# Performance work log

Measured on AMD Instinct MI355X. Metric: run time of the kernel, lower is better.

Reference implementation:

```python
import jax, jax.numpy as jnp
import numpy as np

B, S, I, H = 128, 1024, 512, 1024


def setup_inputs() -> dict:
    key = jax.random.key(0)
    k0, k1, k2 = jax.random.split(key, 3)
    scale = 0.02
    return {
        "x": jax.random.normal(k0, (B, S, I), jnp.float32),
        "feature_weighting": jnp.ones((1, 1, I), jnp.float32),
        "temporal_weighting": jnp.ones((1, S, 1), jnp.float32),
        "magnitude": jnp.ones((1,), jnp.float32),
        "W0": jax.random.normal(k1, (3 * H, I + H), jnp.float32) * scale,
        "b0": jnp.zeros((3 * H,), jnp.float32),
        "W1": jax.random.normal(k2, (3 * H, 2 * H), jnp.float32) * scale,
        "b1": jnp.zeros((3 * H,), jnp.float32),
    }


def _cell(x_t, h_prev, c_prev, W, b):
    # gates: [B, 3H] from cat(x, h_prev) @ W.T + b
    gates = jnp.concatenate([x_t, h_prev], axis=1) @ W.T + b
    i, g, o = jnp.split(gates, 3, axis=1)
    f = jax.nn.sigmoid(c_prev)            # note: forget gate from c_prev (module's quirk)
    c_new = f * c_prev + jax.nn.sigmoid(i) * jnp.tanh(g)
    h_new = jax.nn.sigmoid(o) * jnp.tanh(c_new) * f  # extra *f (module's quirk)
    return h_new, c_new


def reference(x, feature_weighting, temporal_weighting, magnitude, W0, b0, W1, b1):
    batch = x.shape[0]
    hid = W0.shape[0] // 3
    x = x * feature_weighting * temporal_weighting * jnp.exp(magnitude)
    zeros = jnp.zeros((batch, hid), x.dtype)
    init = (zeros, zeros, zeros, zeros)  # h0, c0, h1, c1

    def step(carry, x_t):
        h0, c0, h1, c1 = carry
        h0, c0 = _cell(x_t, h0, c0, W0, b0)
        h1, c1 = _cell(h0, h1, c1, W1, b1)
        return (h0, c0, h1, c1), h1

    (h0, c0, h1, c1), ys = jax.lax.scan(step, init, jnp.swapaxes(x, 0, 1))
    outputs = jnp.swapaxes(ys, 0, 1)  # [B, S, H]
    return outputs, ((h0, c0), (h1, c1))
```

## Files before the change

### kernel.cpp

```cpp
#include <hip/hip_runtime.h>
#include <hip/hip_bf16.h>


typedef __attribute__((ext_vector_type(8))) _Float16 f16x8;
typedef __attribute__((ext_vector_type(4))) float f32x4;
typedef unsigned long long u64;
#define DEV __device__ __forceinline__

namespace {
constexpr int Bb = 128, Ss = 1024, Ii = 512, Hh = 1024;
constexpr int K0 = Ii + Hh;
constexpr int K1 = 2 * Hh;
constexpr int NWG = 256;
constexpr int NPH = Ss + 1;
constexpr int RING = 16;
constexpr int LAG  = 12;
constexpr int SSTR = 32;

constexpr size_t BH    = (size_t)Bb * Hh;
constexpr size_t OF_H0 = (size_t)Bb * Ss * Hh;
constexpr size_t OF_C0 = OF_H0 + BH;
constexpr size_t OF_H1 = OF_C0 + BH;
constexpr size_t OF_C1 = OF_H1 + BH;

constexpr size_t WS_SLOTS = 4096;
constexpr size_t WS_C0    = 40960;
constexpr size_t WS_C1    = WS_C0 + BH * 4;
constexpr size_t RINGF    = (size_t)RING * BH * 2;
constexpr size_t WS_H0F   = WS_C1 + BH * 4;
constexpr size_t WS_H1F   = WS_H0F + RINGF;
constexpr size_t WS_ZEND  = WS_H1F + RINGF;
constexpr size_t WSZ_W0   = (size_t)3 * Hh * K0 * 2;
constexpr size_t WSZ_W1   = (size_t)3 * Hh * K1 * 2;
constexpr size_t WS_W0F   = WS_ZEND;
constexpr size_t WS_W1F   = WS_W0F + WSZ_W0;
constexpr size_t WS_NEED  = WS_W1F + WSZ_W1;

constexpr int CHUNKB    = 3072;
constexpr int LO_BYTES  = 48 * CHUNKB;
constexpr int RED_BYTES = 4 * 3 * 64 * 16;
constexpr int DYN_LDS   = LO_BYTES + RED_BYTES;
}

DEV unsigned short f16b(float f) {
  return __builtin_bit_cast(unsigned short, (_Float16)f);
}
DEV float sig_(float x) { return 1.f / (1.f + __expf(-x)); }
DEV float tanh_(float x) {
  float e = __expf(-2.f * fabsf(x));
  return copysignf((1.f - e) / (1.f + e), x);
}
DEV f16x8 ldh(const unsigned short* p) { return *reinterpret_cast<const f16x8*>(p); }
#define MFMAH __builtin_amdgcn_mfma_f32_16x16x32_f16

__global__ void k_zero(uint4* p, int n16) {
  for (int i = blockIdx.x * blockDim.x + threadIdx.x; i < n16; i += gridDim.x * blockDim.x)
    p[i] = make_uint4(0u, 0u, 0u, 0u);
}

__global__ void k_convert(const float* __restrict__ W0, const float* __restrict__ W1,
                          unsigned short* __restrict__ w0f, unsigned short* __restrict__ w1f) {
  const long NW04 = (long)3 * Hh * K0 / 4;
  const long NW14 = (long)3 * Hh * K1 / 4;
  const long total = NW04 + NW14;
  for (long i = (long)blockIdx.x * blockDim.x + threadIdx.x; i < total;
       i += (long)gridDim.x * blockDim.x) {
    long e; const float* src; unsigned short* dst;
    if (i < NW04) { e = i * 4;          src = W0 + e; dst = w0f + e; }
    else          { e = (i - NW04) * 4; src = W1 + e; dst = w1f + e; }
    f32x4 v = *(const f32x4*)src;
    u64 pk = 0;
#pragma unroll
    for (int e2 = 0; e2 < 4; ++e2) pk |= (u64)f16b(v[e2]) << (16 * e2);
    *(u64*)dst = pk;
  }
}

#define LD_WC(g, ch)                                                          \
  (*(const f16x8*)(lds + (ch) * CHUNKB + (g) * 1024 + l4 * 256 + l15 * 16))

#define HLOAD(arr, n, hP, kaB)                                                \
  _Pragma("unroll") for (int c_ = 0; c_ < (n); ++c_)                          \
    arr[c_] = ldh((hP) + (kaB) + c_ * 32);

#define HCOMP(arr, n, cB)                                                     \
  _Pragma("unroll") for (int c_ = 0; c_ < (n); ++c_) {                        \
    f32x4 &I_ = (c_ & 1) ? aI1 : aI0;                                         \
    f32x4 &G_ = (c_ & 1) ? aG1 : aG0;                                         \
    f32x4 &O_ = (c_ & 1) ? aO1 : aO0;                                         \
    I_ = MFMAH(LD_WC(0, (cB) + c_), arr[c_], I_, 0, 0, 0);                    \
    G_ = MFMAH(LD_WC(1, (cB) + c_), arr[c_], G_, 0, 0, 0);                    \
    O_ = MFMAH(LD_WC(2, (cB) + c_), arr[c_], O_, 0, 0, 0);                    \
  }

#define WLOAD(a0, a1, a2, n, koB)                                             \
  _Pragma("unroll") for (int c_ = 0; c_ < (n); ++c_) {                        \
    const int ko_ = (koB) + c_ * 32;                                          \
    a0[c_] = ldh(wf + off0 + ko_);                                            \
    a1[c_] = ldh(wf + off1 + ko_);                                            \
    a2[c_] = ldh(wf + off2 + ko_);                                            \
  }

#define GCOMP(h_, a0, a1, a2, n)                                              \
  _Pragma("unroll") for (int c_ = 0; c_ < (n); ++c_) {                        \
    f32x4 &I_ = (c_ & 1) ? aI1 : aI0;                                         \
    f32x4 &G_ = (c_ & 1) ? aG1 : aG0;                                         \
    f32x4 &O_ = (c_ & 1) ? aO1 : aO0;                                         \
    I_ = MFMAH(a0[c_], h_[c_], I_, 0, 0, 0);                                  \
    G_ = MFMAH(a1[c_], h_[c_], G_, 0, 0, 0);                                  \
    O_ = MFMAH(a2[c_], h_[c_], O_, 0, 0, 0);                                  \
  }

#define XPREF8(tn)                                                            \
  do {                                                                        \
    const float* pxn_ = xf + ((size_t)bact * Ss + (tn)) * Ii + khk + l4 * 8;  \
    const float twn_ = tw[tn] * emag;                                         \
    _Pragma("unroll") for (int c_ = 0; c_ < 8; ++c_) {                        \
      const int k_ = c_ * 32;                                                 \
      f32x4 a0_ = *(const f32x4*)(pxn_ + k_);                                 \
      f32x4 a1_ = *(const f32x4*)(pxn_ + k_ + 4);                             \
      f32x4 b0_ = *(const f32x4*)(fw + khk + k_ + l4 * 8);                    \
      f32x4 b1_ = *(const f32x4*)(fw + khk + k_ + l4 * 8 + 4);                \
      a0_ *= b0_ * twn_; a1_ *= b1_ * twn_;                                   \
      _Pragma("unroll") for (int e_ = 0; e_ < 4; ++e_) {                      \
        xp[c_][e_] = (_Float16)a0_[e_];                                       \
        xp[c_][e_ + 4] = (_Float16)a1_[e_];                                   \
      }                                                                       \
    }                                                                         \
  } while (0)

#define XCOMP8() HCOMP(xp, 8, khc)

#define ZACC() do { f32x4 z_ = {0.f,0.f,0.f,0.f};                             \
    aI0 = z_; aG0 = z_; aO0 = z_; aI1 = z_; aG1 = z_; aO1 = z_; } while (0)

__global__ __launch_bounds__(512, 1) void lstm_persist(
    const float* __restrict__ xf,
    const float* __restrict__ fw, const float* __restrict__ tw, const float* __restrict__ mag,
    const unsigned short* __restrict__ w0f, const float* __restrict__ b0,
    const unsigned short* __restrict__ w1f, const float* __restrict__ b1,
    float* __restrict__ out,
    unsigned short* __restrict__ h0f, unsigned short* __restrict__ h1f,
    float* __restrict__ c0, float* __restrict__ c1,
    int* __restrict__ slots) {
  extern __shared__ char lds[];
  f32x4* red = reinterpret_cast<f32x4*>(lds + LO_BYTES);

  const int tid = threadIdx.x;
  const int lane = tid & 63;
  const int wv = tid >> 6;
  const int mt = wv & 3;
  const int kh = wv >> 2;
  const int l15 = lane & 15, l4 = lane >> 4;
  const int khk = kh * 256;
  const int khc = kh * 8;

  const int wg = blockIdx.x;
  const int layer = wg >> 7;
  const int i = wg & 127;
  const int x8 = i & 7;
  const int kk = i >> 3;
  const int mg = x8 >> 2;
  const int jt = (x8 & 3) * 16 + kk;
  const int jb = jt * 16;

  const int dom  = layer * 2 + mg;
  const int pdom = layer ? mg : 2 + mg;
  const int idx  = (x8 & 3) * 16 + kk;

  const int bact = mg * 64 + mt * 16 + l15;
  const int j0 = jb + l4 * 4;

  const int K = layer ? K1 : K0;
  const int KB = layer ? 512 : 0;
  const unsigned short* wf = layer ? w1f : w0f;
  const size_t off0 = (size_t)(0 * Hh + jb + l15) * K + l4 * 8;
  const size_t off1 = (size_t)(1 * Hh + jb + l15) * K + l4 * 8;
  const size_t off2 = (size_t)(2 * Hh + jb + l15) * K + l4 * 8;

  const float* bb = layer ? b1 : b0;
  const f32x4 bi = *(const f32x4*)(bb + j0);
  const f32x4 bg = *(const f32x4*)(bb + Hh + j0);
  const f32x4 bo = *(const f32x4*)(bb + 2 * Hh + j0);

  float* cst = (layer ? c1 : c0) + (size_t)bact * Hh + j0;
  float* outb = out + (size_t)bact * Ss * Hh + j0;
  const float emag = __expf(mag[0]);

  {
    const u64* wsl = (const u64*)wf;
    const int K4 = K >> 2;
    const int cb4 = KB >> 2;
    for (int q = tid; q < 48 * 384; q += 512) {
      int R = q / 384;
      int o = q - R * 384;
      int g = R >> 4, rr = R & 15;
      u64 v = wsl[(size_t)(g * Hh + jb + rr) * K4 + cb4 + o];
      *(u64*)(lds + (o >> 3) * CHUNKB + g * 1024 + ((o >> 1) & 3) * 256 +
              rr * 16 + (o & 1) * 8) = v;
    }
  }
  __syncthreads();

  f32x4 aI0, aG0, aO0, aI1, aG1, aO1;
  ZACC();
  f16x8 xp[8];
  if (layer == 0) { XPREF8(0); XCOMP8(); }

  for (int p = 0; p < NPH; ++p) {
    const bool act = layer ? (p >= 1) : (p < Ss);
    const int t = layer ? (p - 1) : p;
    const int rslot = (p - 1) & (RING - 1);
    const int wslot = p & (RING - 1);

    if (act) {
      const unsigned short* hr =
          (layer ? h1f : h0f) + (size_t)rslot * BH + (size_t)bact * Hh + l4 * 8;
      if (kh == 0) {
        f16x8 hA[8], hB[8];
        HLOAD(hA, 8, hr, 0); HLOAD(hB, 8, hr, 256);
        HCOMP(hA, 8, 16); HCOMP(hB, 8, 24);
      } else {
        f16x8 hA[8], hB[8];
        HLOAD(hA, 8, hr, 512); HLOAD(hB, 8, hr, 768);
        HCOMP(hA, 8, 32); HCOMP(hB, 8, 40);
      }

      if (kh == 1) {
        red[((mt * 3 + 0) << 6) + lane] = aI0 + aI1;
        red[((mt * 3 + 1) << 6) + lane] = aG0 + aG1;
        red[((mt * 3 + 2) << 6) + lane] = aO0 + aO1;
      }
      __syncthreads();
      if (kh == 0) {
        f32x4 ai = aI0 + aI1 + red[((mt * 3 + 0) << 6) + lane] + bi;
        f32x4 ag = aG0 + aG1 + red[((mt * 3 + 1) << 6) + lane] + bg;
        f32x4 ao = aO0 + aO1 + red[((mt * 3 + 2) << 6) + lane] + bo;
        f32x4 cp = *(const f32x4*)cst;
        f32x4 cn, hn;
        u64 hpk = 0;
#pragma unroll
        for (int r = 0; r < 4; ++r) {
          float f = sig_(cp[r]);
          float cc = f * cp[r] + sig_(ai[r]) * tanh_(ag[r]);
          float hh = sig_(ao[r]) * tanh_(cc) * f;
          cn[r] = cc; hn[r] = hh;
          hpk |= (u64)f16b(hh) << (16 * r);
        }
        *(f32x4*)cst = cn;
        const size_t wbase = (size_t)wslot * BH + (size_t)bact * Hh + j0;
        __hip_atomic_store((u64*)((layer ? h1f : h0f) + wbase), hpk,
                           __ATOMIC_RELAXED, __HIP_MEMORY_SCOPE_AGENT);
        if (layer) {
          *(f32x4*)(outb + (size_t)t * Hh) = hn;
          if (t == Ss - 1) {
            *(f32x4*)(out + OF_H1 + (size_t)bact * Hh + j0) = hn;
            *(f32x4*)(out + OF_C1 + (size_t)bact * Hh + j0) = cn;
          }
        } else if (t == Ss - 1) {
          *(f32x4*)(out + OF_H0 + (size_t)bact * Hh + j0) = hn;
          *(f32x4*)(out + OF_C0 + (size_t)bact * Hh + j0) = cn;
        }
      }
    }

    if (p < NPH - 1) {
      __syncthreads();
      if ((p & (RING - 1)) == (RING - 1)) {
        if (tid == 0) __builtin_amdgcn_fence(__ATOMIC_ACQUIRE, "agent");
        __syncthreads();
      }
      if (tid == 0)
        __hip_atomic_store(&slots[(dom * 64 + idx) * SSTR], p + 1,
                           __ATOMIC_RELAXED, __HIP_MEMORY_SCOPE_AGENT);

      if (layer == 1) {
        bool ok = (tid >= 64);
        int gd = 0;
        do {
          if (!ok)
            ok = __hip_atomic_load(&slots[(pdom * 64 + tid) * SSTR],
                                   __ATOMIC_RELAXED,
                                   __HIP_MEMORY_SCOPE_AGENT) >= p + 1;
          if (!ok) __builtin_amdgcn_s_sleep(2);
        } while (!__syncthreads_and(ok) && ++gd < (1 << 22));
        ZACC();
        const unsigned short* h0n =
            h0f + (size_t)(p & (RING - 1)) * BH + (size_t)bact * Hh + l4 * 8;
        if (kh == 0) {
          {
            f16x8 sh[6], sA[6], sB[6], sC[6];
            HLOAD(sh, 6, h0n, 0); WLOAD(sA, sB, sC, 6, 0);
            GCOMP(sh, sA, sB, sC, 6);
          }
          {
            f16x8 sh[6], sA[6], sB[6], sC[6];
            HLOAD(sh, 6, h0n, 192); WLOAD(sA, sB, sC, 6, 192);
            GCOMP(sh, sA, sB, sC, 6);
          }
          {
            f16x8 sh[4], sA[4], sB[4], sC[4];
            HLOAD(sh, 4, h0n, 384); WLOAD(sA, sB, sC, 4, 384);
            GCOMP(sh, sA, sB, sC, 4);
          }
        } else {
          f16x8 hA[8], hB[8];
          HLOAD(hA, 8, h0n, 512); HLOAD(hB, 8, h0n, 768);
          HCOMP(hA, 8, 0); HCOMP(hB, 8, 8);
        }
        ok = (tid >= 64);
        gd = 0;
        do {
          if (!ok)
            ok = __hip_atomic_load(&slots[(dom * 64 + tid) * SSTR],
                                   __ATOMIC_RELAXED,
                                   __HIP_MEMORY_SCOPE_AGENT) >= p + 1;
          if (!ok) __builtin_amdgcn_s_sleep(2);
        } while (!__syncthreads_and(ok) && ++gd < (1 << 22));
      } else {
        if (p + 1 < Ss) { XPREF8(p + 1); ZACC(); XCOMP8(); }
        const int pthr = p + 1 - LAG;
        bool ok;
        if (tid < 64)        ok = false;
        else if (tid < 128)  ok = (pthr <= 0);
        else                 ok = true;
        int gd = 0;
        do {
          if (!ok) {
            int v = (tid < 64)
                ? __hip_atomic_load(&slots[(dom * 64 + tid) * SSTR],
                                    __ATOMIC_RELAXED, __HIP_MEMORY_SCOPE_AGENT)
                : __hip_atomic_load(&slots[(pdom * 64 + (tid - 64)) * SSTR],
                                    __ATOMIC_RELAXED, __HIP_MEMORY_SCOPE_AGENT);
            ok = v >= ((tid < 64) ? (p + 1) : pthr);
          }
          if (!ok) __builtin_amdgcn_s_sleep(2);
        } while (!__syncthreads_and(ok) && ++gd < (1 << 22));
      }
    }
  }
}

extern "C" void kernel_launch(void* const* d_in, const int* in_sizes, int n_in,
                              void* d_out, int out_size, void* d_ws, size_t ws_size,
                              hipStream_t stream) {
  const float* x   = (const float*)d_in[0];
  const float* fw  = (const float*)d_in[1];
  const float* tw  = (const float*)d_in[2];
  const float* mag = (const float*)d_in[3];
  const float* W0  = (const float*)d_in[4];
  const float* b0  = (const float*)d_in[5];
  const float* W1  = (const float*)d_in[6];
  const float* b1  = (const float*)d_in[7];
  float* out = (float*)d_out;
  char* ws = (char*)d_ws;

  if (ws_size < WS_NEED) return;

  unsigned short* w0f = (unsigned short*)(ws + WS_W0F);
  unsigned short* w1f = (unsigned short*)(ws + WS_W1F);

  (void)hipFuncSetAttribute((const void*)lstm_persist,
                            hipFuncAttributeMaxDynamicSharedMemorySize, DYN_LDS);

  k_zero<<<2048, 256, 0, stream>>>((uint4*)ws, (int)(WS_ZEND / 16));
  k_convert<<<1024, 256, 0, stream>>>(W0, W1, w0f, w1f);

  lstm_persist<<<NWG, 512, DYN_LDS, stream>>>(
      x, fw, tw, mag, w0f, b0, w1f, b1, out,
      (unsigned short*)(ws + WS_H0F), (unsigned short*)(ws + WS_H1F),
      (float*)(ws + WS_C0), (float*)(ws + WS_C1),
      (int*)(ws + WS_SLOTS));
}
```

Baseline: 16.17 ms.

## Poll barrier flags in one wavefront and shrink the h-ring and layer lag

Replaces the block-wide __syncthreads_and polling loops with single-wavefront polling helpers (poll1/poll2) using __all and a shorter sleep, followed by a plain __syncthreads. This is meant to cut the per-step cost of inter-workgroup synchronization. It also shrinks the hidden-state ring from 16 to 4 slots and the layer lag from 12 to 2, regroups the layer-1 input-part GEMM into two 8-wide chunks instead of 6/6/4, and launches fewer blocks for the zeroing kernel. A smaller ring and lag reduce the memory that has to be zeroed and may keep h buffers hotter in cache, but they tighten the coupling between the two layers, so more stalls are possible.

```diff
diff --git a/kernel.cpp b/kernel.cpp
--- a/kernel.cpp
+++ b/kernel.cpp
@@ -13,8 +13,8 @@
 constexpr int K1 = 2 * Hh;
 constexpr int NWG = 256;
 constexpr int NPH = Ss + 1;
-constexpr int RING = 16;
-constexpr int LAG  = 12;
+constexpr int RING = 4;
+constexpr int LAG  = 2;
 constexpr int SSTR = 32;
 
 constexpr size_t BH    = (size_t)Bb * Hh;
@@ -52,6 +52,30 @@
 }
 DEV f16x8 ldh(const unsigned short* p) { return *reinterpret_cast<const f16x8*>(p); }
 #define MFMAH __builtin_amdgcn_mfma_f32_16x16x32_f16
+
+DEV void poll1(const int* slots, int base, int thr, int lane) {
+  bool ok = false;
+  for (int gd = 0; gd < (1 << 24); ++gd) {
+    if (!ok)
+      ok = __hip_atomic_load(&slots[(base + lane) * SSTR], __ATOMIC_RELAXED,
+                             __HIP_MEMORY_SCOPE_AGENT) >= thr;
+    if (__all(ok)) break;
+    __builtin_amdgcn_s_sleep(1);
+  }
+}
+DEV void poll2(const int* slots, int b1, int t1, int b2, int t2, int lane) {
+  bool ok1 = false, ok2 = (t2 <= 0);
+  for (int gd = 0; gd < (1 << 24); ++gd) {
+    if (!ok1)
+      ok1 = __hip_atomic_load(&slots[(b1 + lane) * SSTR], __ATOMIC_RELAXED,
+                              __HIP_MEMORY_SCOPE_AGENT) >= t1;
+    if (!ok2)
+      ok2 = __hip_atomic_load(&slots[(b2 + lane) * SSTR], __ATOMIC_RELAXED,
+                              __HIP_MEMORY_SCOPE_AGENT) >= t2;
+    if (__all(ok1 && ok2)) break;
+    __builtin_amdgcn_s_sleep(1);
+  }
+}
 
 __global__ void k_zero(uint4* p, int n16) {
   for (int i = blockIdx.x * blockDim.x + threadIdx.x; i < n16; i += gridDim.x * blockDim.x)
@@ -275,67 +299,33 @@
                            __ATOMIC_RELAXED, __HIP_MEMORY_SCOPE_AGENT);
 
       if (layer == 1) {
-        bool ok = (tid >= 64);
-        int gd = 0;
-        do {
-          if (!ok)
-            ok = __hip_atomic_load(&slots[(pdom * 64 + tid) * SSTR],
-                                   __ATOMIC_RELAXED,
-                                   __HIP_MEMORY_SCOPE_AGENT) >= p + 1;
-          if (!ok) __builtin_amdgcn_s_sleep(2);
-        } while (!__syncthreads_and(ok) && ++gd < (1 << 22));
+        if (wv == 0) poll1(slots, pdom * 64, p + 1, lane);
+        __syncthreads();
         ZACC();
         const unsigned short* h0n =
             h0f + (size_t)(p & (RING - 1)) * BH + (size_t)bact * Hh + l4 * 8;
         if (kh == 0) {
           {
-            f16x8 sh[6], sA[6], sB[6], sC[6];
-            HLOAD(sh, 6, h0n, 0); WLOAD(sA, sB, sC, 6, 0);
-            GCOMP(sh, sA, sB, sC, 6);
+            f16x8 sh[8], sA[8], sB[8], sC[8];
+            HLOAD(sh, 8, h0n, 0); WLOAD(sA, sB, sC, 8, 0);
+            GCOMP(sh, sA, sB, sC, 8);
           }
           {
-            f16x8 sh[6], sA[6], sB[6], sC[6];
-            HLOAD(sh, 6, h0n, 192); WLOAD(sA, sB, sC, 6, 192);
-            GCOMP(sh, sA, sB, sC, 6);
-          }
-          {
-            f16x8 sh[4], sA[4], sB[4], sC[4];
-            HLOAD(sh, 4, h0n, 384); WLOAD(sA, sB, sC, 4, 384);
-            GCOMP(sh, sA, sB, sC, 4);
+            f16x8 sh[8], sA[8], sB[8], sC[8];
+            HLOAD(sh, 8, h0n, 256); WLOAD(sA, sB, sC, 8, 256);
+            GCOMP(sh, sA, sB, sC, 8);
           }
         } else {
           f16x8 hA[8], hB[8];
           HLOAD(hA, 8, h0n, 512); HLOAD(hB, 8, h0n, 768);
           HCOMP(hA, 8, 0); HCOMP(hB, 8, 8);
         }
-        ok = (tid >= 64);
-        gd = 0;
-        do {
-          if (!ok)
-            ok = __hip_atomic_load(&slots[(dom * 64 + tid) * SSTR],
-                                   __ATOMIC_RELAXED,
-                                   __HIP_MEMORY_SCOPE_AGENT) >= p + 1;
-          if (!ok) __builtin_amdgcn_s_sleep(2);
-        } while (!__syncthreads_and(ok) && ++gd < (1 << 22));
+        if (wv == 0) poll1(slots, dom * 64, p + 1, lane);
+        __syncthreads();
       } else {
         if (p + 1 < Ss) { XPREF8(p + 1); ZACC(); XCOMP8(); }
-        const int pthr = p + 1 - LAG;
-        bool ok;
-        if (tid < 64)        ok = false;
-        else if (tid < 128)  ok = (pthr <= 0);
-        else                 ok = true;
-        int gd = 0;
-        do {
-          if (!ok) {
-            int v = (tid < 64)
-                ? __hip_atomic_load(&slots[(dom * 64 + tid) * SSTR],
-                                    __ATOMIC_RELAXED, __HIP_MEMORY_SCOPE_AGENT)
-                : __hip_atomic_load(&slots[(pdom * 64 + (tid - 64)) * SSTR],
-                                    __ATOMIC_RELAXED, __HIP_MEMORY_SCOPE_AGENT);
-            ok = v >= ((tid < 64) ? (p + 1) : pthr);
-          }
-          if (!ok) __builtin_amdgcn_s_sleep(2);
-        } while (!__syncthreads_and(ok) && ++gd < (1 << 22));
+        if (wv == 0) poll2(slots, dom * 64, p + 1, pdom * 64, p + 1 - LAG, lane);
+        __syncthreads();
       }
     }
   }
@@ -363,7 +353,7 @@
   (void)hipFuncSetAttribute((const void*)lstm_persist,
                             hipFuncAttributeMaxDynamicSharedMemorySize, DYN_LDS);
 
-  k_zero<<<2048, 256, 0, stream>>>((uint4*)ws, (int)(WS_ZEND / 16));
+  k_zero<<<768, 256, 0, stream>>>((uint4*)ws, (int)(WS_ZEND / 16));
   k_convert<<<1024, 256, 0, stream>>>(W0, W1, w0f, w1f);
 
   lstm_persist<<<NWG, 512, DYN_LDS, stream>>>(
```

Result: faster. 15.46 ms (-4.4%).
